# Kernel optimization log

Hardware: AMD Instinct MI355X
Metric: run time of the kernel (lower is better)

The kernel has to match this reference:

```python
import math
import jax, jax.numpy as jnp
import numpy as np

T_LEN, BSZ, E_DIM, N_HEADS = 2048, 4, 768, 12


def setup_inputs() -> dict:
    key = jax.random.key(0)
    k0, k1, k2 = jax.random.split(key, 3)
    E = E_DIM
    return {
        "query": jax.random.normal(k0, (T_LEN, BSZ, E), dtype=jnp.float32),
        "attn_mask": jnp.zeros((T_LEN, T_LEN), dtype=jnp.float32),
        "in_proj_weight": jax.random.normal(k1, (3 * E, E), dtype=jnp.float32) * (1.0 / math.sqrt(E)),
        "in_proj_bias": jnp.zeros((3 * E,), dtype=jnp.float32),
        "out_proj_weight": jax.random.normal(k2, (E, E), dtype=jnp.float32) * (1.0 / math.sqrt(E)),
        "out_proj_bias": jnp.zeros((E,), dtype=jnp.float32),
        "num_heads": N_HEADS,
    }


def _rope_tables(seq_len, head_dim, dtype):
    # position_enc[pos, j] = pos / 10000**(2j/head_dim), j in [0, head_dim//2)
    pos = jnp.arange(seq_len, dtype=jnp.float32)[:, None]
    j = jnp.arange(head_dim // 2, dtype=jnp.float32)[None, :]
    ang = pos / jnp.power(jnp.float32(10000.0), 2.0 * j / head_dim)
    # stack([x, x], -1).reshape == repeat-interleave by 2 along last dim
    sin = jnp.repeat(jnp.sin(ang), 2, axis=-1).astype(dtype)  # (S, hd)
    cos = jnp.repeat(jnp.cos(ang), 2, axis=-1).astype(dtype)
    return sin, cos


def _rotate_half(x):
    # interleaved pairs: (x0, x1, x2, x3, ...) -> (-x1, x0, -x3, x2, ...)
    x_even = x[..., 0::2]
    x_odd = x[..., 1::2]
    return jnp.stack([-x_odd, x_even], axis=-1).reshape(x.shape)


def reference(query, attn_mask, in_proj_weight, in_proj_bias, out_proj_weight, out_proj_bias, num_heads):
    T, B, E = query.shape
    H = num_heads
    hd = E // H

    # fused QKV in-projection: (T, B, 3E)
    proj = jnp.einsum('tbe,fe->tbf', query, in_proj_weight) + in_proj_bias
    q, k, v = jnp.split(proj, 3, axis=-1)  # each (T, B, E)

    def to_bhtd(x):
        return jnp.transpose(x.reshape(T, B, H, hd), (1, 2, 0, 3))  # (B, H, T, hd)

    q, k, v = to_bhtd(q), to_bhtd(k), to_bhtd(v)

    sin, cos = _rope_tables(T, hd, q.dtype)  # (T, hd), broadcast over (B, H)
    q = q * cos + _rotate_half(q) * sin
    k = k * cos + _rotate_half(k) * sin

    scale = 1.0 / math.sqrt(hd)
    scores = jnp.einsum('bhtd,bhsd->bhts', q, k) * scale + attn_mask[None, None, :, :]
    attn = jax.nn.softmax(scores, axis=-1)
    out = jnp.einsum('bhts,bhsd->bhtd', attn, v)  # (B, H, T, hd)

    out = jnp.transpose(out, (2, 0, 1, 3)).reshape(T * B, E)  # (T*B, E)
    out = out @ out_proj_weight.T + out_proj_bias
    return out.reshape(T, B, E)
```

## Files before the change

kernel.cpp:

```cpp
#include <hip/hip_runtime.h>
#include <math.h>

#define TLEN 2048
#define BSZ  4
#define EDIM 768
#define NH   12
#define HD   64
#define NBH  (BSZ * NH)
#define LOG2E 1.44269504088896f

typedef __bf16 bf16;
typedef __bf16 bf16x8 __attribute__((ext_vector_type(8)));
typedef float  f32x4  __attribute__((ext_vector_type(4)));
typedef unsigned int uint;

__device__ __forceinline__ f32x4 mfma16(bf16x8 a, bf16x8 b, f32x4 c) {
  return __builtin_amdgcn_mfma_f32_16x16x32_bf16(a, b, c, 0, 0, 0);
}

__device__ __forceinline__ uint cvtpk(float lo, float hi) {
  uint r;
  asm("v_cvt_pk_bf16_f32 %0, %1, %2" : "=v"(r) : "v"(lo), "v"(hi));
  return r;
}

#define GLD16(gp, lp)                                                          \
  __builtin_amdgcn_global_load_lds(                                            \
      (const __attribute__((address_space(1))) uint32_t*)(gp),                 \
      (__attribute__((address_space(3))) uint32_t*)(lp), 16, 0, 0)

__device__ __forceinline__ bf16x8 ldsfrag(const bf16* t, int row, int kb) {
  return *reinterpret_cast<const bf16x8*>(
      (const char*)t + row * 128 + (kb ^ ((row & 7) << 4)));
}

__device__ __forceinline__ uint2 ldsfrag64(const bf16* t, int row, int kb) {
  return *reinterpret_cast<const uint2*>(
      (const char*)t + row * 128 + (kb ^ ((row & 7) << 4)));
}

#define CT_OFF   0x0u
#define ST_OFF   0x40000u
#define FLG_OFF  0x80000u
#define AQ_OFF   0x100000u
#define VT_OFF   0x100000u
#define QB_OFF   0xD00000u
#define KB_OFF   0x1900000u
#define VB_OFF   0x2500000u
#define XB_OFF   0x2500000u
#define WI_OFF   0x3100000u
#define WO_OFF   0x3460000u

#define QN8  786432
#define WIN8 221184
#define WON8 73728

__device__ __forceinline__ void cvt8(const float* __restrict__ s,
                                     bf16* __restrict__ d, int i) {
  const float4* sp = reinterpret_cast<const float4*>(s) + (size_t)i * 2;
  float4 a = sp[0], b = sp[1];
  bf16x8 o;
  o[0] = (bf16)a.x; o[1] = (bf16)a.y; o[2] = (bf16)a.z; o[3] = (bf16)a.w;
  o[4] = (bf16)b.x; o[5] = (bf16)b.y; o[6] = (bf16)b.z; o[7] = (bf16)b.w;
  reinterpret_cast<bf16x8*>(d)[i] = o;
}

__global__ __launch_bounds__(256) void prep_all_kernel(
    const float* __restrict__ q, bf16* __restrict__ qo,
    const float* __restrict__ wi, bf16* __restrict__ wio,
    const float* __restrict__ wo, bf16* __restrict__ woo,
    const float* __restrict__ mask, uint* __restrict__ flags,
    float* __restrict__ ct, float* __restrict__ st) {
  int bid = blockIdx.x;
  int tid = threadIdx.x;
  if (bid < 256) {
    int i = bid * 256 + tid;
    int t = i >> 5, j = i & 31;
    double ang = (double)t * pow(10000.0, -(double)j / 32.0);
    st[i] = (float)sin(ang);
    ct[i] = (float)cos(ang);
  } else if (bid < 4480) {
    int i = (bid - 256) * 256 + tid;
    if (i < QN8) { cvt8(q, qo, i); return; }
    int j = i - QN8;
    if (j < WIN8) { cvt8(wi, wio, j); return; }
    cvt8(wo, woo, j - WIN8);
  } else {
    int tile = bid - 4480;
    int ty = tile >> 5, tx = tile & 31;
    uint acc = 0;
#pragma unroll
    for (int i = 0; i < 4; ++i) {
      int c = tid + 256 * i;
      int rr = c >> 4, cc = (c & 15) * 4;
      float4 v = *reinterpret_cast<const float4*>(
          mask + (size_t)(ty * 64 + rr) * TLEN + tx * 64 + cc);
      acc |= __float_as_uint(v.x) | __float_as_uint(v.y) |
             __float_as_uint(v.z) | __float_as_uint(v.w);
    }
    unsigned long long b = __ballot(acc != 0);
    __shared__ uint red[4];
    if ((tid & 63) == 0) red[tid >> 6] = (b != 0ull) ? 1u : 0u;
    __syncthreads();
    if (tid == 0) flags[tile] = red[0] | red[1] | red[2] | red[3];
  }
}

__global__ __launch_bounds__(256) void vtrans_kernel(const bf16* __restrict__ v,
                                                     bf16* __restrict__ vt) {
  int w = threadIdx.x >> 6, lane = threadIdx.x & 63;
  int bh = blockIdx.y;
  int t0 = (blockIdx.x * 4 + w) * 64;
  const bf16* src = v + ((size_t)bh * TLEN + t0) * HD;
  bf16* dst = vt + (size_t)bh * HD * TLEN + t0;
  int d0 = (lane & 7) * 8, tr = (lane >> 3) * 8;
  bf16x8 in[8];
#pragma unroll
  for (int r = 0; r < 8; ++r)
    in[r] = *reinterpret_cast<const bf16x8*>(src + (size_t)(tr + r) * HD + d0);
  bf16x8 out[8];
#pragma unroll
  for (int j = 0; j < 8; ++j)
#pragma unroll
    for (int r = 0; r < 8; ++r) out[j][r] = in[r][j];
#pragma unroll
  for (int j = 0; j < 8; ++j)
    *reinterpret_cast<bf16x8*>(dst + (size_t)(d0 + j) * TLEN + tr) = out[j];
}

template <int MODE>
__global__ __launch_bounds__(256) void gemm_bt(
    const bf16* __restrict__ A, const bf16* __restrict__ B,
    const float* __restrict__ bias,
    const float* __restrict__ ct, const float* __restrict__ st,
    bf16* __restrict__ qo, bf16* __restrict__ ko, bf16* __restrict__ vo,
    float* __restrict__ fo) {
  constexpr int K = EDIM;
  __shared__ __align__(16) bf16 As[128 * 64];
  __shared__ __align__(16) bf16 Bs[128 * 64];
  int tid = threadIdx.x;
  int lane = tid & 63, w = tid >> 6;
  int wr = w >> 1, wc = w & 1;
  int g = lane >> 4, cl = lane & 15;
  int bm = blockIdx.y, bn = blockIdx.x;
  int lrow = lane >> 3;
  int colb = ((lane & 7) ^ lrow) << 4;
  const char* Abase = (const char*)(A + (size_t)bm * 128 * K);
  const char* Bbase = (const char*)(B + (size_t)bn * 128 * K);

  f32x4 acc[4][4] = {};

  for (int kt = 0; kt < K; kt += 64) {
#pragma unroll
    for (int i = 0; i < 4; ++i) {
      int qi = w * 4 + i;
      int row = qi * 8 + lrow;
      GLD16(Abase + (size_t)row * (K * 2) + kt * 2 + colb, As + qi * 512 + lane * 8);
      GLD16(Bbase + (size_t)row * (K * 2) + kt * 2 + colb, Bs + qi * 512 + lane * 8);
    }
    __syncthreads();
#pragma unroll
    for (int kk = 0; kk < 2; ++kk) {
      bf16x8 af[4], bfr[4];
#pragma unroll
      for (int mi = 0; mi < 4; ++mi)
        af[mi] = ldsfrag(As, wr * 64 + mi * 16 + cl, kk * 64 + g * 16);
#pragma unroll
      for (int ni = 0; ni < 4; ++ni)
        bfr[ni] = ldsfrag(Bs, wc * 64 + ni * 16 + cl, kk * 64 + g * 16);
#pragma unroll
      for (int mi = 0; mi < 4; ++mi)
#pragma unroll
        for (int ni = 0; ni < 4; ++ni)
          acc[mi][ni] = mfma16(af[mi], bfr[ni], acc[mi][ni]);
    }
    __syncthreads();
  }

  if (MODE == 0) {
#pragma unroll
    for (int mi = 0; mi < 4; ++mi) {
      int mbase = bm * 128 + wr * 64 + mi * 16 + 4 * g;
      int t = mbase >> 2;
#pragma unroll
      for (int ni = 0; ni < 4; ++ni) {
        int f = bn * 128 + wc * 64 + ni * 16 + cl;
        int sec = f / EDIM;
        int f0 = f - sec * EDIM;
        int h = f0 >> 6, d = f0 & 63;
        float bv = bias[f];
        float vals[4];
#pragma unroll
        for (int r = 0; r < 4; ++r) vals[r] = acc[mi][ni][r] + bv;
        if (sec < 2) {
          int j = d >> 1;
          float cv = ct[t * 32 + j], sv = st[t * 32 + j];
          bf16* dst = (sec == 0) ? qo : ko;
#pragma unroll
          for (int r = 0; r < 4; ++r) {
            float other = __shfl_xor(vals[r], 1);
            float rv = (d & 1) ? (vals[r] * cv + other * sv)
                               : (vals[r] * cv - other * sv);
            if (sec == 0) rv *= 0.125f * LOG2E;
            dst[(((size_t)r * NH + h) * TLEN + t) * HD + d] = (bf16)rv;
          }
        } else {
#pragma unroll
          for (int r = 0; r < 4; ++r)
            vo[(((size_t)r * NH + h) * TLEN + t) * HD + d] = (bf16)vals[r];
        }
      }
    }
  } else {
#pragma unroll
    for (int mi = 0; mi < 4; ++mi) {
      int mbase = bm * 128 + wr * 64 + mi * 16 + 4 * g;
#pragma unroll
      for (int ni = 0; ni < 4; ++ni) {
        int n = bn * 128 + wc * 64 + ni * 16 + cl;
        float bv = bias[n];
#pragma unroll
        for (int r = 0; r < 4; ++r)
          fo[(size_t)(mbase + r) * EDIM + n] = acc[mi][ni][r] + bv;
      }
    }
  }
}

__global__ __launch_bounds__(512) void attn_kernel(
    const bf16* __restrict__ qa, const bf16* __restrict__ ka,
    const bf16* __restrict__ vt, const float* __restrict__ mask,
    const uint* __restrict__ flags, bf16* __restrict__ xo) {
  __shared__ __align__(16) bf16 Ks[2][4096];
  __shared__ __align__(16) bf16 Vs[2][4096];
  int tid = threadIdx.x;
  int lane = tid & 63, w = tid >> 6;
  int g = lane >> 4, cl = lane & 15;
  int bh = blockIdx.y;
  int qrow0 = blockIdx.x * 128 + w * 16;
  const bf16* qbh = qa + (size_t)bh * TLEN * HD;
  const char* kbase = (const char*)(ka + (size_t)bh * TLEN * HD);
  const char* vbase = (const char*)(vt + (size_t)bh * HD * TLEN);
  int lrow = lane >> 3;
  int colb = ((lane & 7) ^ lrow) << 4;
  int sw = w & 3;
  const uint* flgrow = flags + (qrow0 >> 6) * 32;

  bf16x8 qf[2];
#pragma unroll
  for (int h = 0; h < 2; ++h)
    qf[h] = *reinterpret_cast<const bf16x8*>(
        qbh + (size_t)(qrow0 + cl) * HD + h * 32 + g * 8);

  bf16x8 ones;
#pragma unroll
  for (int j = 0; j < 8; ++j) ones[j] = (bf16)1.0f;

  f32x4 o[4] = {};
  f32x4 oden = {};
  float mrow = -1e30f;

#pragma unroll
  for (int i = 0; i < 2; ++i) {
    int qi = sw * 2 + i;
    int row = qi * 8 + lrow;
    if (w < 4)
      GLD16(kbase + (size_t)row * 128 + colb, &Ks[0][qi * 512 + lane * 8]);
    else
      GLD16(vbase + (size_t)row * (TLEN * 2) + colb, &Vs[0][qi * 512 + lane * 8]);
  }
  __syncthreads();

  for (int stile = 0; stile < TLEN / 64; ++stile) {
    int cur = stile & 1;
    if (stile + 1 < TLEN / 64) {
      int s1 = (stile + 1) * 64;
#pragma unroll
      for (int i = 0; i < 2; ++i) {
        int qi = sw * 2 + i;
        int row = qi * 8 + lrow;
        if (w < 4)
          GLD16(kbase + (size_t)(s1 + row) * 128 + colb,
                &Ks[cur ^ 1][qi * 512 + lane * 8]);
        else
          GLD16(vbase + (size_t)row * (TLEN * 2) + s1 * 2 + colb,
                &Vs[cur ^ 1][qi * 512 + lane * 8]);
      }
    }
    const bf16* Kc = Ks[cur];
    const bf16* Vc = Vs[cur];

    f32x4 sc[4];
#pragma unroll
    for (int ni = 0; ni < 4; ++ni) {
      bf16x8 k0 = ldsfrag(Kc, ni * 16 + cl, g * 16);
      bf16x8 k1 = ldsfrag(Kc, ni * 16 + cl, 64 + g * 16);
      f32x4 z = {};
      z = mfma16(k0, qf[0], z);
      z = mfma16(k1, qf[1], z);
      sc[ni] = z;
    }

    if (flgrow[stile]) {
      int q = qrow0 + cl;
#pragma unroll
      for (int ni = 0; ni < 4; ++ni)
#pragma unroll
        for (int r = 0; r < 4; ++r)
          sc[ni][r] = fmaf(mask[(size_t)q * TLEN + stile * 64 + ni * 16 + 4 * g + r],
                           LOG2E, sc[ni][r]);
    }

    float ml = fmaxf(fmaxf(fmaxf(sc[0][0], sc[0][1]), fmaxf(sc[0][2], sc[0][3])),
                     fmaxf(fmaxf(sc[1][0], sc[1][1]), fmaxf(sc[1][2], sc[1][3])));
    ml = fmaxf(ml,
               fmaxf(fmaxf(fmaxf(sc[2][0], sc[2][1]), fmaxf(sc[2][2], sc[2][3])),
                     fmaxf(fmaxf(sc[3][0], sc[3][1]), fmaxf(sc[3][2], sc[3][3]))));
    if (!__all(ml <= mrow + 11.54f)) {
      float mfull = fmaxf(ml, __shfl_xor(ml, 16));
      mfull = fmaxf(mfull, __shfl_xor(mfull, 32));
      float mn = fmaxf(mrow, mfull);
      float al = exp2f(mrow - mn);
      mrow = mn;
#pragma unroll
      for (int di = 0; di < 4; ++di)
#pragma unroll
        for (int r = 0; r < 4; ++r) o[di][r] *= al;
#pragma unroll
      for (int r = 0; r < 4; ++r) oden[r] *= al;
    }

    union { uint u[4]; bf16x8 v; } f0, f1;
#pragma unroll
    for (int ni = 0; ni < 4; ++ni) {
      float p0 = exp2f(sc[ni][0] - mrow);
      float p1 = exp2f(sc[ni][1] - mrow);
      float p2 = exp2f(sc[ni][2] - mrow);
      float p3 = exp2f(sc[ni][3] - mrow);
      uint lo = cvtpk(p0, p1);
      uint hi2 = cvtpk(p2, p3);
      if (ni < 2) { f0.u[2 * ni] = lo; f0.u[2 * ni + 1] = hi2; }
      else        { f1.u[2 * (ni - 2)] = lo; f1.u[2 * (ni - 2) + 1] = hi2; }
    }

#pragma unroll
    for (int di = 0; di < 4; ++di) {
      int row = di * 16 + cl;
      union { uint2 h[2]; bf16x8 v; } va, vb;
      va.h[0] = ldsfrag64(Vc, row, 8 * g);
      va.h[1] = ldsfrag64(Vc, row, 32 + 8 * g);
      vb.h[0] = ldsfrag64(Vc, row, 64 + 8 * g);
      vb.h[1] = ldsfrag64(Vc, row, 96 + 8 * g);
      o[di] = mfma16(va.v, f0.v, o[di]);
      o[di] = mfma16(vb.v, f1.v, o[di]);
    }
    oden = mfma16(ones, f0.v, oden);
    oden = mfma16(ones, f1.v, oden);

    __syncthreads();
  }

  int b = bh / NH, h = bh % NH;
  int t = qrow0 + cl;
  float inv = 1.0f / oden[0];
  bf16* dst = xo + (size_t)(t * BSZ + b) * EDIM + h * HD + 4 * g;
#pragma unroll
  for (int di = 0; di < 4; ++di) {
    union { bf16 hh[4]; uint2 u; } w4;
#pragma unroll
    for (int r = 0; r < 4; ++r) w4.hh[r] = (bf16)(o[di][r] * inv);
    *reinterpret_cast<uint2*>(dst + di * 16) = w4.u;
  }
}

extern "C" void kernel_launch(void* const* d_in, const int* in_sizes, int n_in,
                              void* d_out, int out_size, void* d_ws, size_t ws_size,
                              hipStream_t stream) {
  const float* query = (const float*)d_in[0];
  const float* mask  = (const float*)d_in[1];
  const float* win   = (const float*)d_in[2];
  const float* bin   = (const float*)d_in[3];
  const float* wout  = (const float*)d_in[4];
  const float* bout  = (const float*)d_in[5];
  (void)in_sizes; (void)n_in; (void)out_size; (void)ws_size;

  char* ws = (char*)d_ws;
  float* ct   = (float*)(ws + CT_OFF);
  float* st   = (float*)(ws + ST_OFF);
  uint*  flg  = (uint*)(ws + FLG_OFF);
  bf16*  aq   = (bf16*)(ws + AQ_OFF);
  bf16*  vtb  = (bf16*)(ws + VT_OFF);
  bf16*  qb   = (bf16*)(ws + QB_OFF);
  bf16*  kb   = (bf16*)(ws + KB_OFF);
  bf16*  vb   = (bf16*)(ws + VB_OFF);
  bf16*  xb   = (bf16*)(ws + XB_OFF);
  bf16*  wib  = (bf16*)(ws + WI_OFF);
  bf16*  wob  = (bf16*)(ws + WO_OFF);
  float* out  = (float*)d_out;

  prep_all_kernel<<<dim3(5504), dim3(256), 0, stream>>>(
      query, aq, win, wib, wout, wob, mask, flg, ct, st);

  gemm_bt<0><<<dim3(3 * EDIM / 128, TLEN * BSZ / 128), dim3(256), 0, stream>>>(
      aq, wib, bin, ct, st, qb, kb, vb, nullptr);

  vtrans_kernel<<<dim3(TLEN / 256, NBH), dim3(256), 0, stream>>>(vb, vtb);

  attn_kernel<<<dim3(TLEN / 128, NBH), dim3(512), 0, stream>>>(
      qb, kb, vtb, mask, flg, xb);

  gemm_bt<1><<<dim3(EDIM / 128, TLEN * BSZ / 128), dim3(256), 0, stream>>>(
      xb, wob, bout, nullptr, nullptr, nullptr, nullptr, nullptr, out);
}
```

Baseline: 290.0 us.

## Permute V-transpose column order for 128-bit LDS reads and swizzle attention block order

The V transpose kernel now writes each row of transposed V in a permuted key order. This lets the attention PV step fetch each V fragment with one 128-bit LDS load instead of two 64-bit loads, and the permutation is matched to how the P fragment packs keys. The attention grid is also remapped so that neighbouring workgroups are spread across (batch, head) pairs, which is meant to even out L2/cache usage. The cost is 64-bit scattered global stores in the transpose, and correctness depends on the permutation exactly matching the P fragment layout.

```diff
diff --git a/kernel.cpp b/kernel.cpp
--- a/kernel.cpp
+++ b/kernel.cpp
@@ -31,11 +31,6 @@
 
 __device__ __forceinline__ bf16x8 ldsfrag(const bf16* t, int row, int kb) {
   return *reinterpret_cast<const bf16x8*>(
-      (const char*)t + row * 128 + (kb ^ ((row & 7) << 4)));
-}
-
-__device__ __forceinline__ uint2 ldsfrag64(const bf16* t, int row, int kb) {
-  return *reinterpret_cast<const uint2*>(
       (const char*)t + row * 128 + (kb ^ ((row & 7) << 4)));
 }
 
@@ -113,19 +108,22 @@
   int t0 = (blockIdx.x * 4 + w) * 64;
   const bf16* src = v + ((size_t)bh * TLEN + t0) * HD;
   bf16* dst = vt + (size_t)bh * HD * TLEN + t0;
-  int d0 = (lane & 7) * 8, tr = (lane >> 3) * 8;
+  int d0 = (lane & 7) * 8, a = lane >> 3;
   bf16x8 in[8];
 #pragma unroll
   for (int r = 0; r < 8; ++r)
-    in[r] = *reinterpret_cast<const bf16x8*>(src + (size_t)(tr + r) * HD + d0);
-  bf16x8 out[8];
-#pragma unroll
-  for (int j = 0; j < 8; ++j)
-#pragma unroll
-    for (int r = 0; r < 8; ++r) out[j][r] = in[r][j];
-#pragma unroll
-  for (int j = 0; j < 8; ++j)
-    *reinterpret_cast<bf16x8*>(dst + (size_t)(d0 + j) * TLEN + tr) = out[j];
+    in[r] = *reinterpret_cast<const bf16x8*>(src + (size_t)(8 * a + r) * HD + d0);
+  int p0 = 32 * (a >> 2) + 8 * ((2 * a) & 3) + 4 * ((a >> 1) & 1);
+  int p1 = 32 * (a >> 2) + 8 * ((2 * a + 1) & 3) + 4 * ((a >> 1) & 1);
+#pragma unroll
+  for (int j = 0; j < 8; ++j) {
+    union { bf16 h[4]; uint2 u; } w0, w1;
+#pragma unroll
+    for (int r = 0; r < 4; ++r) { w0.h[r] = in[r][j]; w1.h[r] = in[r + 4][j]; }
+    bf16* rowp = dst + (size_t)(d0 + j) * TLEN;
+    *reinterpret_cast<uint2*>(rowp + p0) = w0.u;
+    *reinterpret_cast<uint2*>(rowp + p1) = w1.u;
+  }
 }
 
 template <int MODE>
@@ -236,8 +234,10 @@
   int tid = threadIdx.x;
   int lane = tid & 63, w = tid >> 6;
   int g = lane >> 4, cl = lane & 15;
-  int bh = blockIdx.y;
-  int qrow0 = blockIdx.x * 128 + w * 16;
+  int lin = blockIdx.y * 16 + blockIdx.x;
+  int lin2 = (lin & 7) * 96 + (lin >> 3);
+  int qt = lin2 & 15, bh = lin2 >> 4;
+  int qrow0 = qt * 128 + w * 16;
   const bf16* qbh = qa + (size_t)bh * TLEN * HD;
   const char* kbase = (const char*)(ka + (size_t)bh * TLEN * HD);
   const char* vbase = (const char*)(vt + (size_t)bh * HD * TLEN);
@@ -346,13 +346,10 @@
 #pragma unroll
     for (int di = 0; di < 4; ++di) {
       int row = di * 16 + cl;
-      union { uint2 h[2]; bf16x8 v; } va, vb;
-      va.h[0] = ldsfrag64(Vc, row, 8 * g);
-      va.h[1] = ldsfrag64(Vc, row, 32 + 8 * g);
-      vb.h[0] = ldsfrag64(Vc, row, 64 + 8 * g);
-      vb.h[1] = ldsfrag64(Vc, row, 96 + 8 * g);
-      o[di] = mfma16(va.v, f0.v, o[di]);
-      o[di] = mfma16(vb.v, f1.v, o[di]);
+      bf16x8 v0 = ldsfrag(Vc, row, g * 16);
+      bf16x8 v1 = ldsfrag(Vc, row, 64 + g * 16);
+      o[di] = mfma16(v0, f0.v, o[di]);
+      o[di] = mfma16(v1, f1.v, o[di]);
     }
     oden = mfma16(ones, f0.v, oden);
     oden = mfma16(ones, f1.v, oden);
```

Result: faster. 278.9 us (-3.8%).
